# Kernel optimization log

Hardware: AMD Instinct MI355X
Metric: run time of the kernel (lower is better)

The kernel has to match this reference:

```python
import jax, jax.numpy as jnp
import numpy as np

BN_EPS = 1e-5


def setup_inputs() -> dict:
    key = jax.random.key(0)
    k1, k2, k3, k4 = jax.random.split(key, 4)
    B, C, H, W = 16, 128, 128, 128
    x = jax.random.normal(k1, (B, C, H, W), dtype=jnp.float32)
    gamma = jax.random.normal(k2, (1,), dtype=jnp.float32)
    bn_weight = jax.random.uniform(k3, (C,), dtype=jnp.float32)
    bn_bias = jax.random.normal(k4, (C,), dtype=jnp.float32)
    return {"x": x, "gamma": gamma, "bn_weight": bn_weight, "bn_bias": bn_bias}


def reference(x, gamma, bn_weight, bn_bias):
    B, C, H, W = x.shape
    q = x.reshape(B, C, H * W)                      # proj_query: [B, C, HW]
    # energy[b, i, j] = <channel i, channel j>
    energy = jnp.einsum('bin,bjn->bij', q, q)       # [B, C, C]
    energy_new = jnp.max(energy, axis=-1, keepdims=True) - energy
    attention = jax.nn.softmax(energy_new, axis=-1)  # [B, C, C]
    out = jnp.einsum('bij,bjn->bin', attention, q)  # [B, C, HW]
    out = out.reshape(B, C, H, W)
    out = gamma * out
    # BatchNorm2d in training mode: batch statistics over (B, H, W) per channel
    mean = jnp.mean(out, axis=(0, 2, 3), keepdims=True)
    var = jnp.var(out, axis=(0, 2, 3), keepdims=True)  # biased variance
    out = (out - mean) * jax.lax.rsqrt(var + BN_EPS)
    out = out * bn_weight[None, :, None, None] + bn_bias[None, :, None, None]
    return out + x
```

## Files before the change

### kernel.cpp

```cpp
#include <hip/hip_runtime.h>

#define BB 16
#define CC 128
#define NN 16384
#define BN_EPS 1e-5f

typedef unsigned short u16;
typedef short short8 __attribute__((ext_vector_type(8)));
typedef float floatx4 __attribute__((ext_vector_type(4)));

__device__ inline float b2f(u16 u) {
    union { unsigned int i; float f; } c; c.i = ((unsigned int)u) << 16; return c.f;
}
__device__ inline u16 f2b(float f) {
    union { float f; unsigned int i; } c; c.f = f;
    unsigned int r = c.i + 0x7fffu + ((c.i >> 16) & 1u);
    return (u16)(r >> 16);
}

#define K1_LD 136
__global__ __launch_bounds__(256) void k_gram(const float* __restrict__ x,
                                              float* __restrict__ part,
                                              float* __restrict__ S)
{
    __shared__ u16 th[128 * K1_LD];
    __shared__ u16 tl[128 * K1_LD];
    __shared__ float rowsum[128];
    const int b     = blockIdx.x >> 4;
    const int chunk = blockIdx.x & 15;
    const int k0    = chunk * 1024;
    const int t     = threadIdx.x;
    const int w = t >> 6, lane = t & 63, quad = lane >> 4, colL = lane & 15;
    if (t < 128) rowsum[t] = 0.f;

    floatx4 acc[2][8];
#pragma unroll
    for (int rt = 0; rt < 2; ++rt)
#pragma unroll
        for (int ct = 0; ct < 8; ++ct) acc[rt][ct] = {0.f, 0.f, 0.f, 0.f};

    const float* xb = x + (size_t)b * CC * NN;
    for (int s = 0; s < 8; ++s) {
        const int ks = k0 + s * 128;
        __syncthreads();
#pragma unroll
        for (int it = 0; it < 16; ++it) {
            int idx = it * 256 + t;
            int row = idx >> 5, c4 = idx & 31;
            float4 v = *(const float4*)(xb + (size_t)row * NN + ks + c4 * 4);
            u16 h0 = f2b(v.x), h1 = f2b(v.y), h2 = f2b(v.z), h3 = f2b(v.w);
            uint2 hv, lv;
            hv.x = (unsigned)h0 | ((unsigned)h1 << 16);
            hv.y = (unsigned)h2 | ((unsigned)h3 << 16);
            lv.x = (unsigned)f2b(v.x - b2f(h0)) | ((unsigned)f2b(v.y - b2f(h1)) << 16);
            lv.y = (unsigned)f2b(v.z - b2f(h2)) | ((unsigned)f2b(v.w - b2f(h3)) << 16);
            *(uint2*)&th[row * K1_LD + c4 * 4] = hv;
            *(uint2*)&tl[row * K1_LD + c4 * 4] = lv;
            float ps = v.x + v.y + v.z + v.w;
#pragma unroll
            for (int off = 16; off > 0; off >>= 1) ps += __shfl_down(ps, off, 32);
            if ((lane & 31) == 0) rowsum[row] += ps;
        }
        __syncthreads();
        const int rbase = w * 32;
#pragma unroll
        for (int ks2 = 0; ks2 < 4; ++ks2) {
            const int kk = ks2 * 32 + quad * 8;
            short8 a0h = *(const short8*)&th[(rbase + colL) * K1_LD + kk];
            short8 a1h = *(const short8*)&th[(rbase + 16 + colL) * K1_LD + kk];
            short8 a0l = *(const short8*)&tl[(rbase + colL) * K1_LD + kk];
            short8 a1l = *(const short8*)&tl[(rbase + 16 + colL) * K1_LD + kk];
#pragma unroll
            for (int ct = 0; ct < 8; ++ct) {
                short8 bh = *(const short8*)&th[(ct * 16 + colL) * K1_LD + kk];
                short8 bl = *(const short8*)&tl[(ct * 16 + colL) * K1_LD + kk];
                acc[0][ct] = __builtin_amdgcn_mfma_f32_16x16x32_bf16(a0h, bh, acc[0][ct], 0, 0, 0);
                acc[1][ct] = __builtin_amdgcn_mfma_f32_16x16x32_bf16(a1h, bh, acc[1][ct], 0, 0, 0);
                acc[0][ct] = __builtin_amdgcn_mfma_f32_16x16x32_bf16(a0l, bh, acc[0][ct], 0, 0, 0);
                acc[1][ct] = __builtin_amdgcn_mfma_f32_16x16x32_bf16(a1l, bh, acc[1][ct], 0, 0, 0);
                acc[0][ct] = __builtin_amdgcn_mfma_f32_16x16x32_bf16(a0h, bl, acc[0][ct], 0, 0, 0);
                acc[1][ct] = __builtin_amdgcn_mfma_f32_16x16x32_bf16(a1h, bl, acc[1][ct], 0, 0, 0);
            }
        }
    }
    float* pb = part + (size_t)(b * 16 + chunk) * CC * CC;
#pragma unroll
    for (int rt = 0; rt < 2; ++rt)
#pragma unroll
        for (int ct = 0; ct < 8; ++ct)
#pragma unroll
            for (int r = 0; r < 4; ++r) {
                int row = w * 32 + rt * 16 + quad * 4 + r;
                int col = ct * 16 + colL;
                pb[row * CC + col] = acc[rt][ct][r];
            }
    __syncthreads();
    if (t < 128) atomicAdd(&S[b * CC + t], rowsum[t]);
}

__global__ __launch_bounds__(256) void k_reduce(const float* __restrict__ part,
                                                float* __restrict__ energy)
{
    int idx = blockIdx.x * 256 + threadIdx.x;
    int b = idx >> 14;
    int ij = idx & 16383;
    const float* p = part + (size_t)b * 16 * 16384 + ij;
    float s = 0.f;
#pragma unroll
    for (int c = 0; c < 16; ++c) s += p[c * 16384];
    energy[idx] = s;
}

__global__ __launch_bounds__(256) void k_soft(const float* __restrict__ energy,
                                              const float* __restrict__ S,
                                              u16* __restrict__ attb,
                                              float* __restrict__ meanacc,
                                              float* __restrict__ e2acc)
{
    const int b = blockIdx.x >> 7;
    const int i = blockIdx.x & 127;
    const int t = threadIdx.x;
    __shared__ float att[128];
    __shared__ float red[256];
    const float* E = energy + b * CC * CC;

    float e = (t < 128) ? E[i * CC + t] : 3.0e38f;
    red[t] = e; __syncthreads();
    for (int s2 = 128; s2 > 0; s2 >>= 1) { if (t < s2) red[t] = fminf(red[t], red[t + s2]); __syncthreads(); }
    float emin = red[0]; __syncthreads();

    float a = (t < 128) ? expf(emin - e) : 0.f;
    red[t] = a; __syncthreads();
    for (int s2 = 128; s2 > 0; s2 >>= 1) { if (t < s2) red[t] += red[t + s2]; __syncthreads(); }
    float Z = red[0]; __syncthreads();

    float attf = 0.f;
    if (t < 128) {
        u16 ab = f2b(a / Z);
        attf = b2f(ab);
        attb[((size_t)b * CC + i) * CC + t] = ab;
        att[t] = attf;
    }
    float mp = (t < 128) ? attf * S[b * CC + t] : 0.f;
    red[t] = mp; __syncthreads();
    for (int s2 = 128; s2 > 0; s2 >>= 1) { if (t < s2) red[t] += red[t + s2]; __syncthreads(); }
    if (t == 0) atomicAdd(&meanacc[i], red[0]);
    __syncthreads();

    const int j    = t & 127;
    const int half = t >> 7;
    const float* Ej = E + j * CC + half * 64;
    float inner = 0.f;
#pragma unroll 8
    for (int k = 0; k < 64; ++k) inner += att[half * 64 + k] * Ej[k];
    red[t] = inner; __syncthreads();
    float contrib = (t < 128) ? (red[t] + red[t + 128]) * att[t] : 0.f;
    __syncthreads();
    red[t] = contrib; __syncthreads();
    for (int s2 = 128; s2 > 0; s2 >>= 1) { if (t < s2) red[t] += red[t + s2]; __syncthreads(); }
    if (t == 0) atomicAdd(&e2acc[i], red[0]);
}

#define K3_LD 136
__global__ __launch_bounds__(256) void k_out(const float* __restrict__ x,
                                             const u16* __restrict__ attb,
                                             const float* __restrict__ meanacc,
                                             const float* __restrict__ e2acc,
                                             const float* __restrict__ gamma,
                                             const float* __restrict__ bnw,
                                             const float* __restrict__ bnb,
                                             float* __restrict__ out)
{
    __shared__ u16 attl[128 * K3_LD];
    __shared__ u16 qbf[128 * K3_LD];
    __shared__ float alpha[128];
    __shared__ float beta[128];
    const int b   = blockIdx.x >> 7;
    const int nn0 = (blockIdx.x & 127) * 128;
    const int t   = threadIdx.x;

    if (t < 128) {
        float g   = gamma[0];
        const float invBN = 1.f / (float)(BB * NN);
        float m   = g * meanacc[t] * invBN;
        float e2  = g * g * e2acc[t] * invBN;
        float var = e2 - m * m;
        float inv = rsqrtf(var + BN_EPS);
        float wv  = bnw[t];
        alpha[t] = g * wv * inv;
        beta[t]  = bnb[t] - m * wv * inv;
    }
    const u16* ab = attb + (size_t)b * CC * CC;
#pragma unroll
    for (int it = 0; it < 8; ++it) {
        int idx = it * 256 + t;
        int row = idx >> 4, c8 = idx & 15;
        *(uint4*)&attl[row * K3_LD + c8 * 8] = *(const uint4*)&ab[row * CC + c8 * 8];
    }
    const float* xb = x + (size_t)b * CC * NN + nn0;
#pragma unroll
    for (int it = 0; it < 16; ++it) {
        int idx = it * 256 + t;
        int row = idx >> 5, c4 = idx & 31;
        float4 v = *(const float4*)(xb + (size_t)row * NN + c4 * 4);
        uint2 hv;
        hv.x = (unsigned)f2b(v.x) | ((unsigned)f2b(v.y) << 16);
        hv.y = (unsigned)f2b(v.z) | ((unsigned)f2b(v.w) << 16);
        *(uint2*)&qbf[row * K3_LD + c4 * 4] = hv;
    }
    __syncthreads();

    const int w = t >> 6, lane = t & 63, quad = lane >> 4, colL = lane & 15;
    floatx4 acc[8][2];
#pragma unroll
    for (int rt = 0; rt < 8; ++rt) { acc[rt][0] = {0.f,0.f,0.f,0.f}; acc[rt][1] = {0.f,0.f,0.f,0.f}; }

#pragma unroll
    for (int ks = 0; ks < 4; ++ks) {
        const int kk = ks * 32 + quad * 8;
        short8 bf0, bf1;
#pragma unroll
        for (int j2 = 0; j2 < 8; ++j2) {
            bf0[j2] = (short)qbf[(kk + j2) * K3_LD + w * 32 + colL];
            bf1[j2] = (short)qbf[(kk + j2) * K3_LD + w * 32 + 16 + colL];
        }
#pragma unroll
        for (int rt = 0; rt < 8; ++rt) {
            short8 af = *(const short8*)&attl[(rt * 16 + colL) * K3_LD + kk];
            acc[rt][0] = __builtin_amdgcn_mfma_f32_16x16x32_bf16(af, bf0, acc[rt][0], 0, 0, 0);
            acc[rt][1] = __builtin_amdgcn_mfma_f32_16x16x32_bf16(af, bf1, acc[rt][1], 0, 0, 0);
        }
    }

    float* ob = out + (size_t)b * CC * NN + nn0;
#pragma unroll
    for (int rt = 0; rt < 8; ++rt)
#pragma unroll
        for (int ct = 0; ct < 2; ++ct)
#pragma unroll
            for (int r = 0; r < 4; ++r) {
                int chn = rt * 16 + quad * 4 + r;
                int nn  = w * 32 + ct * 16 + colL;
                float v = alpha[chn] * acc[rt][ct][r] + beta[chn]
                        + xb[(size_t)chn * NN + nn];
                ob[(size_t)chn * NN + nn] = v;
            }
}

extern "C" void kernel_launch(void* const* d_in, const int* in_sizes, int n_in,
                              void* d_out, int out_size, void* d_ws, size_t ws_size,
                              hipStream_t stream)
{
    const float* x     = (const float*)d_in[0];
    const float* gamma = (const float*)d_in[1];
    const float* bnw   = (const float*)d_in[2];
    const float* bnb   = (const float*)d_in[3];
    float* out = (float*)d_out;

    char* ws = (char*)d_ws;
    float* part    = (float*)(ws);
    float* energy  = (float*)(ws + 16777216);
    float* S       = (float*)(ws + 17825792);
    float* meanacc = (float*)(ws + 17833984);
    float* e2acc   = (float*)(ws + 17834496);
    u16*   attb    = (u16*)(ws + 17835008);

    hipMemsetAsync(ws + 17825792, 0, 9216, stream);
    hipLaunchKernelGGL(k_gram,   dim3(256),  dim3(256), 0, stream, x, part, S);
    hipLaunchKernelGGL(k_reduce, dim3(1024), dim3(256), 0, stream, part, energy);
    hipLaunchKernelGGL(k_soft,   dim3(2048), dim3(256), 0, stream, energy, S, attb, meanacc, e2acc);
    hipLaunchKernelGGL(k_out,    dim3(2048), dim3(256), 0, stream, x, attb, meanacc, e2acc, gamma, bnw, bnb, out);
}
```

Measured before the change: 392.8 us.

## Split Gram kernel finer with atomic accumulation and read attention directly in output kernel

The Gram kernel now runs 1024 blocks, each covering 256 columns, and accumulates partial energies directly into the energy buffer with float atomics. This removes the separate reduction kernel and the large partials buffer. Row sums are kept in registers and reduced with shuffles instead of shared-memory atomics. The output kernel stores x transposed in LDS with a swizzle so B fragments load as vectors, and reads attention fragments straight from global memory, cutting LDS usage to raise occupancy. The costs are many more global atomics and float sums whose order is no longer deterministic.

```diff
diff --git a/kernel.cpp b/kernel.cpp
--- a/kernel.cpp
+++ b/kernel.cpp
@@ -18,35 +18,37 @@
     return (u16)(r >> 16);
 }
 
-#define K1_LD 136
-__global__ __launch_bounds__(256) void k_gram(const float* __restrict__ x,
-                                              float* __restrict__ part,
-                                              float* __restrict__ S)
+#define K1_LD 72
+__global__ __launch_bounds__(256, 4) void k_gram(const float* __restrict__ x,
+                                                 float* __restrict__ energy,
+                                                 float* __restrict__ S)
 {
     __shared__ u16 th[128 * K1_LD];
     __shared__ u16 tl[128 * K1_LD];
-    __shared__ float rowsum[128];
-    const int b     = blockIdx.x >> 4;
-    const int chunk = blockIdx.x & 15;
-    const int k0    = chunk * 1024;
+    const int b     = blockIdx.x >> 6;
+    const int chunk = blockIdx.x & 63;
+    const int k0    = chunk * 256;
     const int t     = threadIdx.x;
     const int w = t >> 6, lane = t & 63, quad = lane >> 4, colL = lane & 15;
-    if (t < 128) rowsum[t] = 0.f;
 
     floatx4 acc[2][8];
 #pragma unroll
     for (int rt = 0; rt < 2; ++rt)
 #pragma unroll
         for (int ct = 0; ct < 8; ++ct) acc[rt][ct] = {0.f, 0.f, 0.f, 0.f};
+    float rs[8];
+#pragma unroll
+    for (int it = 0; it < 8; ++it) rs[it] = 0.f;
 
     const float* xb = x + (size_t)b * CC * NN;
-    for (int s = 0; s < 8; ++s) {
-        const int ks = k0 + s * 128;
+    const int rrow = t >> 4;
+    const int c4   = t & 15;
+    for (int s = 0; s < 4; ++s) {
+        const int ks = k0 + s * 64;
         __syncthreads();
 #pragma unroll
-        for (int it = 0; it < 16; ++it) {
-            int idx = it * 256 + t;
-            int row = idx >> 5, c4 = idx & 31;
+        for (int it = 0; it < 8; ++it) {
+            int row = it * 16 + rrow;
             float4 v = *(const float4*)(xb + (size_t)row * NN + ks + c4 * 4);
             u16 h0 = f2b(v.x), h1 = f2b(v.y), h2 = f2b(v.z), h3 = f2b(v.w);
             uint2 hv, lv;
@@ -56,15 +58,12 @@
             lv.y = (unsigned)f2b(v.z - b2f(h2)) | ((unsigned)f2b(v.w - b2f(h3)) << 16);
             *(uint2*)&th[row * K1_LD + c4 * 4] = hv;
             *(uint2*)&tl[row * K1_LD + c4 * 4] = lv;
-            float ps = v.x + v.y + v.z + v.w;
-#pragma unroll
-            for (int off = 16; off > 0; off >>= 1) ps += __shfl_down(ps, off, 32);
-            if ((lane & 31) == 0) rowsum[row] += ps;
+            rs[it] += (v.x + v.y) + (v.z + v.w);
         }
         __syncthreads();
         const int rbase = w * 32;
 #pragma unroll
-        for (int ks2 = 0; ks2 < 4; ++ks2) {
+        for (int ks2 = 0; ks2 < 2; ++ks2) {
             const int kk = ks2 * 32 + quad * 8;
             short8 a0h = *(const short8*)&th[(rbase + colL) * K1_LD + kk];
             short8 a1h = *(const short8*)&th[(rbase + 16 + colL) * K1_LD + kk];
@@ -83,7 +82,7 @@
             }
         }
     }
-    float* pb = part + (size_t)(b * 16 + chunk) * CC * CC;
+    float* eb = energy + b * CC * CC;
 #pragma unroll
     for (int rt = 0; rt < 2; ++rt)
 #pragma unroll
@@ -92,23 +91,15 @@
             for (int r = 0; r < 4; ++r) {
                 int row = w * 32 + rt * 16 + quad * 4 + r;
                 int col = ct * 16 + colL;
-                pb[row * CC + col] = acc[rt][ct][r];
+                atomicAdd(&eb[row * CC + col], acc[rt][ct][r]);
             }
-    __syncthreads();
-    if (t < 128) atomicAdd(&S[b * CC + t], rowsum[t]);
-}
-
-__global__ __launch_bounds__(256) void k_reduce(const float* __restrict__ part,
-                                                float* __restrict__ energy)
-{
-    int idx = blockIdx.x * 256 + threadIdx.x;
-    int b = idx >> 14;
-    int ij = idx & 16383;
-    const float* p = part + (size_t)b * 16 * 16384 + ij;
-    float s = 0.f;
-#pragma unroll
-    for (int c = 0; c < 16; ++c) s += p[c * 16384];
-    energy[idx] = s;
+#pragma unroll
+    for (int it = 0; it < 8; ++it) {
+        float ps = rs[it];
+#pragma unroll
+        for (int off = 8; off > 0; off >>= 1) ps += __shfl_down(ps, off, 16);
+        if (colL == 0) atomicAdd(&S[b * CC + it * 16 + w * 4 + quad], ps);
+    }
 }
 
 __global__ __launch_bounds__(256) void k_soft(const float* __restrict__ energy,
@@ -162,17 +153,16 @@
 }
 
 #define K3_LD 136
-__global__ __launch_bounds__(256) void k_out(const float* __restrict__ x,
-                                             const u16* __restrict__ attb,
-                                             const float* __restrict__ meanacc,
-                                             const float* __restrict__ e2acc,
-                                             const float* __restrict__ gamma,
-                                             const float* __restrict__ bnw,
-                                             const float* __restrict__ bnb,
-                                             float* __restrict__ out)
-{
-    __shared__ u16 attl[128 * K3_LD];
-    __shared__ u16 qbf[128 * K3_LD];
+__global__ __launch_bounds__(256, 4) void k_out(const float* __restrict__ x,
+                                                const u16* __restrict__ attb,
+                                                const float* __restrict__ meanacc,
+                                                const float* __restrict__ e2acc,
+                                                const float* __restrict__ gamma,
+                                                const float* __restrict__ bnw,
+                                                const float* __restrict__ bnb,
+                                                float* __restrict__ out)
+{
+    __shared__ u16 qT[128 * K3_LD];
     __shared__ float alpha[128];
     __shared__ float beta[128];
     const int b   = blockIdx.x >> 7;
@@ -190,27 +180,35 @@
         alpha[t] = g * wv * inv;
         beta[t]  = bnb[t] - m * wv * inv;
     }
-    const u16* ab = attb + (size_t)b * CC * CC;
-#pragma unroll
-    for (int it = 0; it < 8; ++it) {
-        int idx = it * 256 + t;
-        int row = idx >> 4, c8 = idx & 15;
-        *(uint4*)&attl[row * K3_LD + c8 * 8] = *(const uint4*)&ab[row * CC + c8 * 8];
-    }
+
     const float* xb = x + (size_t)b * CC * NN + nn0;
-#pragma unroll
-    for (int it = 0; it < 16; ++it) {
-        int idx = it * 256 + t;
-        int row = idx >> 5, c4 = idx & 31;
-        float4 v = *(const float4*)(xb + (size_t)row * NN + c4 * 4);
-        uint2 hv;
-        hv.x = (unsigned)f2b(v.x) | ((unsigned)f2b(v.y) << 16);
-        hv.y = (unsigned)f2b(v.z) | ((unsigned)f2b(v.w) << 16);
-        *(uint2*)&qbf[row * K3_LD + c4 * 4] = hv;
+    const int n0 = (t & 31) * 4;
+#pragma unroll
+    for (int rep = 0; rep < 4; ++rep) {
+        const int c0 = ((t >> 5) + rep * 8) * 4;
+        float4 f0 = *(const float4*)(xb + (size_t)(c0 + 0) * NN + n0);
+        float4 f1 = *(const float4*)(xb + (size_t)(c0 + 1) * NN + n0);
+        float4 f2 = *(const float4*)(xb + (size_t)(c0 + 2) * NN + n0);
+        float4 f3 = *(const float4*)(xb + (size_t)(c0 + 3) * NN + n0);
+        const float fx[4] = {f0.x, f1.x, f2.x, f3.x};
+        const float fy[4] = {f0.y, f1.y, f2.y, f3.y};
+        const float fz[4] = {f0.z, f1.z, f2.z, f3.z};
+        const float fw[4] = {f0.w, f1.w, f2.w, f3.w};
+        const float* cols[4] = {fx, fy, fz, fw};
+#pragma unroll
+        for (int jn = 0; jn < 4; ++jn) {
+            int n = n0 + jn;
+            int g = ((c0 >> 3) + n) & 15;
+            uint2 v;
+            v.x = (unsigned)f2b(cols[jn][0]) | ((unsigned)f2b(cols[jn][1]) << 16);
+            v.y = (unsigned)f2b(cols[jn][2]) | ((unsigned)f2b(cols[jn][3]) << 16);
+            *(uint2*)&qT[n * K3_LD + g * 8 + (c0 & 7)] = v;
+        }
     }
     __syncthreads();
 
     const int w = t >> 6, lane = t & 63, quad = lane >> 4, colL = lane & 15;
+    const u16* ag = attb + (size_t)b * CC * CC;
     floatx4 acc[8][2];
 #pragma unroll
     for (int rt = 0; rt < 8; ++rt) { acc[rt][0] = {0.f,0.f,0.f,0.f}; acc[rt][1] = {0.f,0.f,0.f,0.f}; }
@@ -218,15 +216,13 @@
 #pragma unroll
     for (int ks = 0; ks < 4; ++ks) {
         const int kk = ks * 32 + quad * 8;
-        short8 bf0, bf1;
-#pragma unroll
-        for (int j2 = 0; j2 < 8; ++j2) {
-            bf0[j2] = (short)qbf[(kk + j2) * K3_LD + w * 32 + colL];
-            bf1[j2] = (short)qbf[(kk + j2) * K3_LD + w * 32 + 16 + colL];
-        }
+        const int n_a = w * 32 + colL;
+        const int n_b = n_a + 16;
+        short8 bf0 = *(const short8*)&qT[n_a * K3_LD + ((((kk) >> 3) + n_a) & 15) * 8];
+        short8 bf1 = *(const short8*)&qT[n_b * K3_LD + ((((kk) >> 3) + n_b) & 15) * 8];
 #pragma unroll
         for (int rt = 0; rt < 8; ++rt) {
-            short8 af = *(const short8*)&attl[(rt * 16 + colL) * K3_LD + kk];
+            short8 af = *(const short8*)&ag[(rt * 16 + colL) * CC + kk];
             acc[rt][0] = __builtin_amdgcn_mfma_f32_16x16x32_bf16(af, bf0, acc[rt][0], 0, 0, 0);
             acc[rt][1] = __builtin_amdgcn_mfma_f32_16x16x32_bf16(af, bf1, acc[rt][1], 0, 0, 0);
         }
@@ -258,16 +254,14 @@
     float* out = (float*)d_out;
 
     char* ws = (char*)d_ws;
-    float* part    = (float*)(ws);
-    float* energy  = (float*)(ws + 16777216);
-    float* S       = (float*)(ws + 17825792);
-    float* meanacc = (float*)(ws + 17833984);
-    float* e2acc   = (float*)(ws + 17834496);
-    u16*   attb    = (u16*)(ws + 17835008);
-
-    hipMemsetAsync(ws + 17825792, 0, 9216, stream);
-    hipLaunchKernelGGL(k_gram,   dim3(256),  dim3(256), 0, stream, x, part, S);
-    hipLaunchKernelGGL(k_reduce, dim3(1024), dim3(256), 0, stream, part, energy);
-    hipLaunchKernelGGL(k_soft,   dim3(2048), dim3(256), 0, stream, energy, S, attb, meanacc, e2acc);
-    hipLaunchKernelGGL(k_out,    dim3(2048), dim3(256), 0, stream, x, attb, meanacc, e2acc, gamma, bnw, bnb, out);
-}
+    float* energy  = (float*)(ws);
+    float* S       = (float*)(ws + 1048576);
+    float* meanacc = (float*)(ws + 1056768);
+    float* e2acc   = (float*)(ws + 1057280);
+    u16*   attb    = (u16*)(ws + 1057792);
+
+    hipMemsetAsync(ws, 0, 1057792, stream);
+    hipLaunchKernelGGL(k_gram, dim3(1024), dim3(256), 0, stream, x, energy, S);
+    hipLaunchKernelGGL(k_soft, dim3(2048), dim3(256), 0, stream, energy, S, attb, meanacc, e2acc);
+    hipLaunchKernelGGL(k_out,  dim3(2048), dim3(256), 0, stream, x, attb, meanacc, e2acc, gamma, bnw, bnb, out);
+}
```

After: 371.0 us. 5.6% less time.
